# Optimization experiments

Measured on AMD Instinct MI355X. Metric: run time of the kernel, lower is better.

Reference implementation:

```python
import jax, jax.numpy as jnp
import numpy as np

SIGMA = 2.5
B, L, V, C = 8, 2048, 8192, 64
F = 2 * (C + 1)  # top_net in_features = 130


def rbf_interp(points_1, feats_1, points_2, sigma):
    """RBF interpolation of feats_1 at points_1 onto points_2 (atom2D torch_rbf, concat=True).
    points_1: [V,3], feats_1: [V,C], points_2: [L,3] -> [L, C+1]
    """
    # exact cdist via gram trick, [L, V]
    d2 = (jnp.sum(points_2 * points_2, -1)[:, None]
          - 2.0 * (points_2 @ points_1.T)
          + jnp.sum(points_1 * points_1, -1)[None, :])
    d = jnp.sqrt(jnp.maximum(d2, 0.0))
    w = jnp.exp(-d / sigma)                       # [L, V]
    dens = jnp.sum(w, axis=1, keepdims=True)      # [L, 1]
    w = w / dens
    # original computes weights under torch.no_grad()
    w = jax.lax.stop_gradient(w)
    dens = jax.lax.stop_gradient(dens)
    feats_2 = w @ feats_1                         # [L, C]
    return jnp.concatenate([feats_2, dens], axis=1)


def setup_inputs() -> dict:
    key = jax.random.key(0)
    ks = jax.random.split(key, 8)
    return {
        "locs_left": jax.random.normal(ks[0], (B, L, 3), jnp.float32),
        "locs_right": jax.random.normal(ks[1], (B, L, 3), jnp.float32),
        "verts_left": jax.random.normal(ks[2], (B, V, 3), jnp.float32),
        "verts_right": jax.random.normal(ks[3], (B, V, 3), jnp.float32),
        "feats_left": jax.random.normal(ks[4], (B, V, C), jnp.float32),
        "feats_right": jax.random.normal(ks[5], (B, V, C), jnp.float32),
        "w1": jax.random.normal(ks[6], (F, F), jnp.float32) * (1.0 / np.sqrt(F)),
        "b1": jnp.zeros((F,), jnp.float32),
        "w2": jax.random.normal(ks[7], (1, F), jnp.float32) * (1.0 / np.sqrt(F)),
        "b2": jnp.zeros((1,), jnp.float32),
    }


def reference(locs_left, locs_right, verts_left, verts_right,
              feats_left, feats_right, w1, b1, w2, b2):
    interp = jax.vmap(lambda p1, f1, p2: rbf_interp(p1, f1, p2, SIGMA))
    fl = interp(verts_left, feats_left, locs_left)     # [B, L, C+1]
    fr = interp(verts_right, feats_right, locs_right)  # [B, L, C+1]
    x = jnp.concatenate([fl, fr], axis=-1)             # [B, L, 2*(C+1)]
    h = jax.nn.relu(x @ w1.T + b1)                     # dropout inactive at eval
    out = h @ w2.T + b2                                # [B, L, 1]
    return out.reshape(-1)                             # [B*L]
```

## Files before the change

### kernel.cpp

```cpp
#include <hip/hip_runtime.h>
#include <hip/hip_bf16.h>
#include <stdint.h>

#define B_ 8
#define L_ 2048
#define V_ 8192
#define C_ 64
#define F_ 130

typedef float    f32x4  __attribute__((ext_vector_type(4)));
typedef float    f32x2  __attribute__((ext_vector_type(2)));
typedef short    s16x8  __attribute__((ext_vector_type(8)));
typedef __bf16   bf16x8 __attribute__((ext_vector_type(8)));
typedef uint32_t u32x4  __attribute__((ext_vector_type(4)));

#if __has_builtin(__builtin_amdgcn_exp2f)
#define EXP2(x) __builtin_amdgcn_exp2f(x)
#else
#define EXP2(x) exp2f(x)
#endif

#if __has_builtin(__builtin_elementwise_fma)
#define PK_FMA4(a,b,c) __builtin_elementwise_fma((a),(b),(c))
#else
__device__ __forceinline__ f32x4 PK_FMA4(f32x4 a, f32x4 b, f32x4 c) {
  f32x4 r; for (int i=0;i<4;++i) r[i]=fmaf(a[i],b[i],c[i]); return r;
}
#endif
#if __has_builtin(__builtin_elementwise_max)
#define PK_MAX4(a,b) __builtin_elementwise_max((a),(b))
#else
__device__ __forceinline__ f32x4 PK_MAX4(f32x4 a, f32x4 b) {
  f32x4 r; for (int i=0;i<4;++i) r[i]=fmaxf(a[i],b[i]); return r;
}
#endif

constexpr float KEXP2 = (float)(0.57707801635558535 * 0.57707801635558535);

__device__ __forceinline__ uint32_t pack2bf(float a, float b) {
  uint16_t ua = __builtin_bit_cast(uint16_t, (__bf16)a);
  uint16_t ub = __builtin_bit_cast(uint16_t, (__bf16)b);
  return (uint32_t)ua | ((uint32_t)ub << 16);
}

__device__ __forceinline__ float wave_sum(float v) {
  v += __shfl_xor(v, 1);  v += __shfl_xor(v, 2);  v += __shfl_xor(v, 4);
  v += __shfl_xor(v, 8);  v += __shfl_xor(v, 16); v += __shfl_xor(v, 32);
  return v;
}

__device__ __forceinline__ void gload_lds16(const void* g, void* l) {
  __builtin_amdgcn_global_load_lds(
      (const __attribute__((address_space(1))) void*)g,
      (__attribute__((address_space(3))) void*)l, 16, 0, 0);
}

__global__ __launch_bounds__(256) void pre_kernel(
    const float* __restrict__ verts_l, const float* __restrict__ verts_r,
    const float* __restrict__ feats_l, const float* __restrict__ feats_r,
    uint16_t* __restrict__ fT2, float* __restrict__ vS2)
{
  __shared__ float fs[64][68];
  const int blk = blockIdx.x, tid = threadIdx.x;
  if (blk < 1024) {
    const int p = blk >> 6, kt2 = blk & 63;
    const int side = p >> 3, bb = p & 7;
    const float* src = (side ? feats_r : feats_l) + (size_t)bb * (V_ * C_);
    #pragma unroll
    for (int sub = 0; sub < 2; ++sub) {
      const int ktile = kt2 * 2 + sub;
      const int v0 = ktile * 64;
      {
        const int sv = tid >> 2, c0 = (tid & 3) * 16;
        const int m = ((sv >> 3) & 7) << 3;
        const float* s = src + (size_t)(v0 + sv) * C_ + c0;
        f32x4 a = *(const f32x4*)(s);
        f32x4 b = *(const f32x4*)(s + 4);
        f32x4 c = *(const f32x4*)(s + 8);
        f32x4 d = *(const f32x4*)(s + 12);
        *(f32x4*)&fs[sv][(c0)      ^ m] = a;
        *(f32x4*)&fs[sv][(c0 + 4)  ^ m] = b;
        *(f32x4*)&fs[sv][(c0 + 8)  ^ m] = c;
        *(f32x4*)&fs[sv][(c0 + 12) ^ m] = d;
      }
      __syncthreads();
      {
        char* tb = (char*)fT2 + ((size_t)p * 128 + ktile) * 8192;
        #pragma unroll
        for (int half = 0; half < 2; ++half) {
          const int r  = half * 256 + tid;
          const int ch = r >> 3;
          const int kq = (r & 7) ^ (ch & 7);
          const int cs = ch ^ (kq << 3);
          const int row0 = kq * 8;
          float f[8];
          #pragma unroll
          for (int e = 0; e < 8; ++e) f[e] = fs[row0 + e][cs];
          u32x4 val = { pack2bf(f[0], f[1]), pack2bf(f[2], f[3]),
                        pack2bf(f[4], f[5]), pack2bf(f[6], f[7]) };
          *(u32x4*)(tb + r * 16) = val;
        }
      }
      __syncthreads();
    }
  } else {
    const int blk2 = blk - 1024;
    const int p = blk2 >> 5, chunk = blk2 & 31;
    const int side = p >> 3, bb = p & 7;
    const float* src = (side ? verts_r : verts_l) + (size_t)bb * (V_ * 3);
    const int v = chunk * 256 + tid;
    const float x = src[v * 3 + 0], y = src[v * 3 + 1], z = src[v * 3 + 2];
    const float n2 = x * x + y * y + z * z;
    constexpr float M2K = -2.0f * KEXP2;
    float* d = vS2 + (size_t)p * 32768 + (size_t)(v >> 6) * 256 + (v & 63);
    d[0] = M2K * x; d[64] = M2K * y; d[128] = M2K * z; d[192] = KEXP2 * n2;
  }
}

__global__ __launch_bounds__(512, 4) void fused_kernel(
    const float* __restrict__ locs_l, const float* __restrict__ locs_r,
    const uint16_t* __restrict__ fT2, const float* __restrict__ vS2,
    const float* __restrict__ w1, const float* __restrict__ b1,
    const float* __restrict__ w2, const float* __restrict__ b2,
    float* __restrict__ outp)
{
  __shared__ __align__(16) char  flds[3][16384];
  __shared__ __align__(16) float vlds[3][2][4][64];
  __shared__ __align__(16) float xs[32][132];
  __shared__ float densp[32];

  const int bid  = blockIdx.x;
  const int bb   = bid & 7;
  const int tile = bid >> 3;
  const int tid  = threadIdx.x;
  const int wid  = tid >> 6, lane = tid & 63;
  const int g    = wid & 1, h = wid >> 1;
  const int ln15 = lane & 15, lg = lane >> 4;
  const int xorv = (ln15 & 7) << 4;
  const f32x4 zero4 = {0.f, 0.f, 0.f, 0.f};

  const int sub  = h >> 1;
  const int hh   = h & 1;
  const int abfix = sub * 8192 + ln15 * 128 + ((((hh << 2) | lg) << 4) ^ xorv);

  for (int s = 0; s < 2; ++s) {
    const int p = s * 8 + bb;
    const float* locs = (s ? locs_r : locs_l) + (size_t)bb * (L_ * 3);
    const int arow = tile * 32 + g * 16 + ln15;
    const float px = locs[arow * 3 + 0];
    const float py = locs[arow * 3 + 1];
    const float pz = locs[arow * 3 + 2];
    const float pn2p = KEXP2 * (px * px + py * py + pz * pz);
    const f32x4 px4 = {px, px, px, px};
    const f32x4 py4 = {py, py, py, py};
    const f32x4 pz4 = {pz, pz, pz, pz};
    const f32x4 pn4 = {pn2p, pn2p, pn2p, pn2p};

    const char* ftp = (const char*)fT2 + (size_t)p * (128 * 8192);
    const char* vtp = (const char*)vS2 + (size_t)p * (128 * 1024);

    f32x4 acc0 = zero4, acc1 = zero4, acc2 = zero4, acc3 = zero4;
    f32x4 densa = zero4;

    gload_lds16(ftp + wid * 2048 + lane * 16,        &flds[0][wid * 2048]);
    gload_lds16(ftp + wid * 2048 + 1024 + lane * 16, &flds[0][wid * 2048 + 1024]);
    if (wid < 2) gload_lds16(vtp + wid * 1024 + lane * 16, &vlds[0][wid][0][0]);

    const char* gfn = ftp + 16384 + wid * 2048 + lane * 16;
    const char* gvn = vtp + 2048  + wid * 1024 + lane * 16;

    int cur = 0, nxt = 1;
    for (int kt = 0; kt < 64; ++kt) {
      if (kt < 63) {
        gload_lds16(gfn,        &flds[nxt][wid * 2048]);
        gload_lds16(gfn + 1024, &flds[nxt][wid * 2048 + 1024]);
        if (wid < 2) {
          gload_lds16(gvn, &vlds[nxt][wid][0][0]);
          asm volatile("s_waitcnt vmcnt(3)" ::: "memory");
        } else {
          asm volatile("s_waitcnt vmcnt(2)" ::: "memory");
        }
        gfn += 16384;
        gvn += 2048;
      } else {
        asm volatile("s_waitcnt vmcnt(0)" ::: "memory");
      }
      __builtin_amdgcn_s_barrier();

      const int kof = hh * 32 + lg * 8;
      const f32x4 vxa = *(const f32x4*)&vlds[cur][sub][0][kof];
      const f32x4 vxb = *(const f32x4*)&vlds[cur][sub][0][kof + 4];
      const f32x4 vya = *(const f32x4*)&vlds[cur][sub][1][kof];
      const f32x4 vyb = *(const f32x4*)&vlds[cur][sub][1][kof + 4];
      const f32x4 vza = *(const f32x4*)&vlds[cur][sub][2][kof];
      const f32x4 vzb = *(const f32x4*)&vlds[cur][sub][2][kof + 4];
      const f32x4 vna = *(const f32x4*)&vlds[cur][sub][3][kof];
      const f32x4 vnb = *(const f32x4*)&vlds[cur][sub][3][kof + 4];

      f32x4 d2a = PK_FMA4(vza, pz4, vna + pn4);
      d2a = PK_FMA4(vya, py4, d2a);
      d2a = PK_FMA4(vxa, px4, d2a);
      d2a = PK_MAX4(d2a, zero4);
      f32x4 d2b = PK_FMA4(vzb, pz4, vnb + pn4);
      d2b = PK_FMA4(vyb, py4, d2b);
      d2b = PK_FMA4(vxb, px4, d2b);
      d2b = PK_MAX4(d2b, zero4);

      f32x4 wa, wb;
      #pragma unroll
      for (int e = 0; e < 4; ++e) {
        wa[e] = EXP2(-__builtin_amdgcn_sqrtf(d2a[e]));
        wb[e] = EXP2(-__builtin_amdgcn_sqrtf(d2b[e]));
      }
      densa += wa;
      densa += wb;
      bf16x8 av;
      #pragma unroll
      for (int e = 0; e < 4; ++e) {
        av[e]     = (__bf16)wa[e];
        av[e + 4] = (__bf16)wb[e];
      }
      const s16x8 afrag = __builtin_bit_cast(s16x8, av);
      const char* fl = flds[cur];
      const s16x8 bf0 = *(const s16x8*)(fl + abfix);
      const s16x8 bf1 = *(const s16x8*)(fl + abfix + 2048);
      const s16x8 bf2 = *(const s16x8*)(fl + abfix + 4096);
      const s16x8 bf3 = *(const s16x8*)(fl + abfix + 6144);
      acc0 = __builtin_amdgcn_mfma_f32_16x16x32_bf16(afrag, bf0, acc0, 0, 0, 0);
      acc1 = __builtin_amdgcn_mfma_f32_16x16x32_bf16(afrag, bf1, acc1, 0, 0, 0);
      acc2 = __builtin_amdgcn_mfma_f32_16x16x32_bf16(afrag, bf2, acc2, 0, 0, 0);
      acc3 = __builtin_amdgcn_mfma_f32_16x16x32_bf16(afrag, bf3, acc3, 0, 0, 0);

      cur = (cur == 2) ? 0 : cur + 1;
      nxt = (nxt == 2) ? 0 : nxt + 1;
    }

    float dens = (densa.x + densa.y) + (densa.z + densa.w);
    dens += __shfl_xor(dens, 16);
    dens += __shfl_xor(dens, 32);

    #pragma unroll
    for (int ph = 0; ph < 4; ++ph) {
      if (h == ph) {
        if (ph == 0) {
          if (lane < 16) densp[g * 16 + lane] = dens;
          #pragma unroll
          for (int r = 0; r < 4; ++r) {
            const int row = g * 16 + lg * 4 + r;
            xs[row][s * 65 +      ln15] = acc0[r];
            xs[row][s * 65 + 16 + ln15] = acc1[r];
            xs[row][s * 65 + 32 + ln15] = acc2[r];
            xs[row][s * 65 + 48 + ln15] = acc3[r];
          }
        } else {
          if (lane < 16) densp[g * 16 + lane] += dens;
          #pragma unroll
          for (int r = 0; r < 4; ++r) {
            const int row = g * 16 + lg * 4 + r;
            xs[row][s * 65 +      ln15] += acc0[r];
            xs[row][s * 65 + 16 + ln15] += acc1[r];
            xs[row][s * 65 + 32 + ln15] += acc2[r];
            xs[row][s * 65 + 48 + ln15] += acc3[r];
          }
        }
      }
      __syncthreads();
    }
    for (int idx = tid; idx < 32 * 64; idx += 512) {
      const int row = idx >> 6, c = idx & 63;
      xs[row][s * 65 + c] *= (1.0f / densp[row]);
    }
    if (tid < 32) xs[tid][s * 65 + 64] = densp[tid];
    __syncthreads();
  }

  const int r0 = wid * 4;
  float hh0[4] = {0.f,0.f,0.f,0.f}, hh1[4] = {0.f,0.f,0.f,0.f};
  const float* wr0 = w1 + (size_t)lane * F_;
  const float* wr1 = w1 + (size_t)(lane + 64) * F_;

  #pragma unroll 4
  for (int i = 0; i < 128; i += 4) {
    const f32x2 a01 = *(const f32x2*)&wr0[i];
    const f32x2 a23 = *(const f32x2*)&wr0[i + 2];
    const f32x2 c01 = *(const f32x2*)&wr1[i];
    const f32x2 c23 = *(const f32x2*)&wr1[i + 2];
    #pragma unroll
    for (int r = 0; r < 4; ++r) {
      const f32x4 xv = *(const f32x4*)&xs[r0 + r][i];
      hh0[r] = fmaf(xv.x, a01.x, hh0[r]); hh0[r] = fmaf(xv.y, a01.y, hh0[r]);
      hh0[r] = fmaf(xv.z, a23.x, hh0[r]); hh0[r] = fmaf(xv.w, a23.y, hh0[r]);
      hh1[r] = fmaf(xv.x, c01.x, hh1[r]); hh1[r] = fmaf(xv.y, c01.y, hh1[r]);
      hh1[r] = fmaf(xv.z, c23.x, hh1[r]); hh1[r] = fmaf(xv.w, c23.y, hh1[r]);
    }
  }
  {
    const float a0 = wr0[128], a1 = wr0[129];
    const float c0 = wr1[128], c1 = wr1[129];
    #pragma unroll
    for (int r = 0; r < 4; ++r) {
      const float x0 = xs[r0 + r][128], x1 = xs[r0 + r][129];
      hh0[r] = fmaf(x0, a0, fmaf(x1, a1, hh0[r]));
      hh1[r] = fmaf(x0, c0, fmaf(x1, c1, hh1[r]));
    }
  }
  const float* wr2 = w1 + 128 * F_;
  const float* wr3 = w1 + 129 * F_;
  float hp2[4], hp3[4];
  #pragma unroll
  for (int r = 0; r < 4; ++r) {
    const float xa = xs[r0 + r][lane];
    const float xb = xs[r0 + r][lane + 64];
    float p2 = wr2[lane] * xa + wr2[lane + 64] * xb;
    float p3 = wr3[lane] * xa + wr3[lane + 64] * xb;
    if (lane < 2) {
      const float xc = xs[r0 + r][128 + lane];
      p2 += wr2[128 + lane] * xc;
      p3 += wr3[128 + lane] * xc;
    }
    hp2[r] = wave_sum(p2);
    hp3[r] = wave_sum(p3);
  }
  const float b1a = b1[lane], b1b = b1[lane + 64];
  const float w2a = w2[lane], w2b = w2[lane + 64];
  const float b1c = b1[128], b1d = b1[129];
  const float w2c = w2[128], w2d = w2[129];
  const float b2v = b2[0];
  #pragma unroll
  for (int r = 0; r < 4; ++r) {
    float o = w2a * fmaxf(hh0[r] + b1a, 0.f) + w2b * fmaxf(hh1[r] + b1b, 0.f);
    o = wave_sum(o);
    if (lane == 0) {
      o += w2c * fmaxf(hp2[r] + b1c, 0.f) + w2d * fmaxf(hp3[r] + b1d, 0.f);
      outp[(size_t)bb * L_ + tile * 32 + r0 + r] = o + b2v;
    }
  }
}

extern "C" void kernel_launch(void* const* d_in, const int* in_sizes, int n_in,
                              void* d_out, int out_size, void* d_ws, size_t ws_size,
                              hipStream_t stream) {
  const float* locs_l  = (const float*)d_in[0];
  const float* locs_r  = (const float*)d_in[1];
  const float* verts_l = (const float*)d_in[2];
  const float* verts_r = (const float*)d_in[3];
  const float* feats_l = (const float*)d_in[4];
  const float* feats_r = (const float*)d_in[5];
  const float* w1 = (const float*)d_in[6];
  const float* b1 = (const float*)d_in[7];
  const float* w2 = (const float*)d_in[8];
  const float* b2 = (const float*)d_in[9];

  char* ws = (char*)d_ws;
  uint16_t* fT2 = (uint16_t*)ws;
  float*    vS2 = (float*)(ws + 16777216);
  float*    out = (float*)d_out;

  pre_kernel<<<1536, 256, 0, stream>>>(verts_l, verts_r, feats_l, feats_r, fT2, vS2);
  fused_kernel<<<512, 512, 0, stream>>>(locs_l, locs_r, fT2, vS2,
                                        w1, b1, w2, b2, out);
}
```

Baseline: 223.7 us.

## Halve block to 4 waves, each wave computing 32 rows to reuse B fragments

Each block now runs 4 waves instead of 8. Each wave handles both 16-row groups of the 32-row tile, so every LDS-loaded feature fragment feeds two MFMA sets. The per-K-tile staging is redistributed across fewer waves, with more async loads per wave and adjusted waitcnt values, and the MLP epilogue processes 8 rows per wave. This cuts LDS fragment reads and wave count per block. In exchange, each wave holds more accumulator registers and does serial weight generation for two row groups, and occupancy changes through the new launch bounds.

```diff
diff --git a/kernel.cpp b/kernel.cpp
--- a/kernel.cpp
+++ b/kernel.cpp
@@ -117,7 +117,7 @@
   }
 }
 
-__global__ __launch_bounds__(512, 4) void fused_kernel(
+__global__ __launch_bounds__(256, 2) void fused_kernel(
     const float* __restrict__ locs_l, const float* __restrict__ locs_r,
     const uint16_t* __restrict__ fT2, const float* __restrict__ vS2,
     const float* __restrict__ w1, const float* __restrict__ b1,
@@ -134,60 +134,89 @@
   const int tile = bid >> 3;
   const int tid  = threadIdx.x;
   const int wid  = tid >> 6, lane = tid & 63;
-  const int g    = wid & 1, h = wid >> 1;
   const int ln15 = lane & 15, lg = lane >> 4;
   const int xorv = (ln15 & 7) << 4;
   const f32x4 zero4 = {0.f, 0.f, 0.f, 0.f};
 
-  const int sub  = h >> 1;
-  const int hh   = h & 1;
+  const int sub  = wid >> 1;
+  const int hh   = wid & 1;
   const int abfix = sub * 8192 + ln15 * 128 + ((((hh << 2) | lg) << 4) ^ xorv);
+  const int kof  = hh * 32 + lg * 8;
 
   for (int s = 0; s < 2; ++s) {
     const int p = s * 8 + bb;
     const float* locs = (s ? locs_r : locs_l) + (size_t)bb * (L_ * 3);
-    const int arow = tile * 32 + g * 16 + ln15;
-    const float px = locs[arow * 3 + 0];
-    const float py = locs[arow * 3 + 1];
-    const float pz = locs[arow * 3 + 2];
-    const float pn2p = KEXP2 * (px * px + py * py + pz * pz);
-    const f32x4 px4 = {px, px, px, px};
-    const f32x4 py4 = {py, py, py, py};
-    const f32x4 pz4 = {pz, pz, pz, pz};
-    const f32x4 pn4 = {pn2p, pn2p, pn2p, pn2p};
-
-    const char* ftp = (const char*)fT2 + (size_t)p * (128 * 8192);
-    const char* vtp = (const char*)vS2 + (size_t)p * (128 * 1024);
-
-    f32x4 acc0 = zero4, acc1 = zero4, acc2 = zero4, acc3 = zero4;
-    f32x4 densa = zero4;
-
-    gload_lds16(ftp + wid * 2048 + lane * 16,        &flds[0][wid * 2048]);
-    gload_lds16(ftp + wid * 2048 + 1024 + lane * 16, &flds[0][wid * 2048 + 1024]);
-    if (wid < 2) gload_lds16(vtp + wid * 1024 + lane * 16, &vlds[0][wid][0][0]);
-
-    const char* gfn = ftp + 16384 + wid * 2048 + lane * 16;
-    const char* gvn = vtp + 2048  + wid * 1024 + lane * 16;
+    const int arow0 = tile * 32 + ln15;
+    const float qx0 = locs[arow0 * 3 + 0];
+    const float qy0 = locs[arow0 * 3 + 1];
+    const float qz0 = locs[arow0 * 3 + 2];
+    const float qx1 = locs[(arow0 + 16) * 3 + 0];
+    const float qy1 = locs[(arow0 + 16) * 3 + 1];
+    const float qz1 = locs[(arow0 + 16) * 3 + 2];
+    const float qn0 = KEXP2 * (qx0 * qx0 + qy0 * qy0 + qz0 * qz0);
+    const float qn1 = KEXP2 * (qx1 * qx1 + qy1 * qy1 + qz1 * qz1);
+    const f32x4 px0 = {qx0,qx0,qx0,qx0}, py0 = {qy0,qy0,qy0,qy0};
+    const f32x4 pz0 = {qz0,qz0,qz0,qz0}, pn0 = {qn0,qn0,qn0,qn0};
+    const f32x4 px1 = {qx1,qx1,qx1,qx1}, py1 = {qy1,qy1,qy1,qy1};
+    const f32x4 pz1 = {qz1,qz1,qz1,qz1}, pn1 = {qn1,qn1,qn1,qn1};
+
+    const char*  ftp = (const char*)fT2 + (size_t)p * (128 * 8192);
+    const char*  vtp = (const char*)vS2 + (size_t)p * (128 * 1024);
+
+    f32x4 a00 = zero4, a01 = zero4, a02 = zero4, a03 = zero4;
+    f32x4 a10 = zero4, a11 = zero4, a12 = zero4, a13 = zero4;
+    f32x4 dac0 = zero4, dac1 = zero4;
+
+    auto stage = [&](int ktile, int buf) {
+      const char* gf = ftp + (size_t)ktile * 16384 + wid * 1024 + lane * 16;
+      if (wid < 2)
+        gload_lds16(vtp + (size_t)ktile * 2048 + wid * 1024 + lane * 16,
+                    &vlds[buf][wid][0][0]);
+      gload_lds16(gf,         &flds[buf][wid * 1024]);
+      gload_lds16(gf + 4096,  &flds[buf][wid * 1024 + 4096]);
+      gload_lds16(gf + 8192,  &flds[buf][wid * 1024 + 8192]);
+      gload_lds16(gf + 12288, &flds[buf][wid * 1024 + 12288]);
+    };
+
+    auto wgen = [&](const f32x4& vxa, const f32x4& vxb, const f32x4& vya,
+                    const f32x4& vyb, const f32x4& vza, const f32x4& vzb,
+                    const f32x4& vna, const f32x4& vnb,
+                    const f32x4& px4, const f32x4& py4, const f32x4& pz4,
+                    const f32x4& pn4, f32x4& dacc) -> s16x8 {
+      f32x4 d2a = PK_FMA4(vza, pz4, vna + pn4);
+      d2a = PK_FMA4(vya, py4, d2a);
+      d2a = PK_FMA4(vxa, px4, d2a);
+      d2a = PK_MAX4(d2a, zero4);
+      f32x4 d2b = PK_FMA4(vzb, pz4, vnb + pn4);
+      d2b = PK_FMA4(vyb, py4, d2b);
+      d2b = PK_FMA4(vxb, px4, d2b);
+      d2b = PK_MAX4(d2b, zero4);
+      f32x4 wa, wb;
+      #pragma unroll
+      for (int e = 0; e < 4; ++e) {
+        wa[e] = EXP2(-__builtin_amdgcn_sqrtf(d2a[e]));
+        wb[e] = EXP2(-__builtin_amdgcn_sqrtf(d2b[e]));
+      }
+      dacc += wa; dacc += wb;
+      bf16x8 av;
+      #pragma unroll
+      for (int e = 0; e < 4; ++e) { av[e] = (__bf16)wa[e]; av[e+4] = (__bf16)wb[e]; }
+      return __builtin_bit_cast(s16x8, av);
+    };
+
+    stage(0, 0);
 
     int cur = 0, nxt = 1;
     for (int kt = 0; kt < 64; ++kt) {
       if (kt < 63) {
-        gload_lds16(gfn,        &flds[nxt][wid * 2048]);
-        gload_lds16(gfn + 1024, &flds[nxt][wid * 2048 + 1024]);
-        if (wid < 2) {
-          gload_lds16(gvn, &vlds[nxt][wid][0][0]);
-          asm volatile("s_waitcnt vmcnt(3)" ::: "memory");
-        } else {
-          asm volatile("s_waitcnt vmcnt(2)" ::: "memory");
-        }
-        gfn += 16384;
-        gvn += 2048;
+        stage(kt + 1, nxt);
+        if (wid < 2) { asm volatile("s_waitcnt vmcnt(5)" ::: "memory"); }
+        else         { asm volatile("s_waitcnt vmcnt(4)" ::: "memory"); }
       } else {
         asm volatile("s_waitcnt vmcnt(0)" ::: "memory");
       }
       __builtin_amdgcn_s_barrier();
 
-      const int kof = hh * 32 + lg * 8;
       const f32x4 vxa = *(const f32x4*)&vlds[cur][sub][0][kof];
       const f32x4 vxb = *(const f32x4*)&vlds[cur][sub][0][kof + 4];
       const f32x4 vya = *(const f32x4*)&vlds[cur][sub][1][kof];
@@ -197,76 +226,71 @@
       const f32x4 vna = *(const f32x4*)&vlds[cur][sub][3][kof];
       const f32x4 vnb = *(const f32x4*)&vlds[cur][sub][3][kof + 4];
 
-      f32x4 d2a = PK_FMA4(vza, pz4, vna + pn4);
-      d2a = PK_FMA4(vya, py4, d2a);
-      d2a = PK_FMA4(vxa, px4, d2a);
-      d2a = PK_MAX4(d2a, zero4);
-      f32x4 d2b = PK_FMA4(vzb, pz4, vnb + pn4);
-      d2b = PK_FMA4(vyb, py4, d2b);
-      d2b = PK_FMA4(vxb, px4, d2b);
-      d2b = PK_MAX4(d2b, zero4);
-
-      f32x4 wa, wb;
-      #pragma unroll
-      for (int e = 0; e < 4; ++e) {
-        wa[e] = EXP2(-__builtin_amdgcn_sqrtf(d2a[e]));
-        wb[e] = EXP2(-__builtin_amdgcn_sqrtf(d2b[e]));
-      }
-      densa += wa;
-      densa += wb;
-      bf16x8 av;
-      #pragma unroll
-      for (int e = 0; e < 4; ++e) {
-        av[e]     = (__bf16)wa[e];
-        av[e + 4] = (__bf16)wb[e];
-      }
-      const s16x8 afrag = __builtin_bit_cast(s16x8, av);
       const char* fl = flds[cur];
       const s16x8 bf0 = *(const s16x8*)(fl + abfix);
       const s16x8 bf1 = *(const s16x8*)(fl + abfix + 2048);
       const s16x8 bf2 = *(const s16x8*)(fl + abfix + 4096);
       const s16x8 bf3 = *(const s16x8*)(fl + abfix + 6144);
-      acc0 = __builtin_amdgcn_mfma_f32_16x16x32_bf16(afrag, bf0, acc0, 0, 0, 0);
-      acc1 = __builtin_amdgcn_mfma_f32_16x16x32_bf16(afrag, bf1, acc1, 0, 0, 0);
-      acc2 = __builtin_amdgcn_mfma_f32_16x16x32_bf16(afrag, bf2, acc2, 0, 0, 0);
-      acc3 = __builtin_amdgcn_mfma_f32_16x16x32_bf16(afrag, bf3, acc3, 0, 0, 0);
+
+      const s16x8 af0 = wgen(vxa,vxb,vya,vyb,vza,vzb,vna,vnb,
+                             px0,py0,pz0,pn0, dac0);
+      a00 = __builtin_amdgcn_mfma_f32_16x16x32_bf16(af0, bf0, a00, 0, 0, 0);
+      a01 = __builtin_amdgcn_mfma_f32_16x16x32_bf16(af0, bf1, a01, 0, 0, 0);
+      a02 = __builtin_amdgcn_mfma_f32_16x16x32_bf16(af0, bf2, a02, 0, 0, 0);
+      a03 = __builtin_amdgcn_mfma_f32_16x16x32_bf16(af0, bf3, a03, 0, 0, 0);
+
+      const s16x8 af1 = wgen(vxa,vxb,vya,vyb,vza,vzb,vna,vnb,
+                             px1,py1,pz1,pn1, dac1);
+      a10 = __builtin_amdgcn_mfma_f32_16x16x32_bf16(af1, bf0, a10, 0, 0, 0);
+      a11 = __builtin_amdgcn_mfma_f32_16x16x32_bf16(af1, bf1, a11, 0, 0, 0);
+      a12 = __builtin_amdgcn_mfma_f32_16x16x32_bf16(af1, bf2, a12, 0, 0, 0);
+      a13 = __builtin_amdgcn_mfma_f32_16x16x32_bf16(af1, bf3, a13, 0, 0, 0);
 
       cur = (cur == 2) ? 0 : cur + 1;
       nxt = (nxt == 2) ? 0 : nxt + 1;
     }
 
-    float dens = (densa.x + densa.y) + (densa.z + densa.w);
-    dens += __shfl_xor(dens, 16);
-    dens += __shfl_xor(dens, 32);
+    float dens0 = (dac0.x + dac0.y) + (dac0.z + dac0.w);
+    float dens1 = (dac1.x + dac1.y) + (dac1.z + dac1.w);
+    dens0 += __shfl_xor(dens0, 16);  dens0 += __shfl_xor(dens0, 32);
+    dens1 += __shfl_xor(dens1, 16);  dens1 += __shfl_xor(dens1, 32);
 
     #pragma unroll
     for (int ph = 0; ph < 4; ++ph) {
-      if (h == ph) {
+      if (wid == ph) {
         if (ph == 0) {
-          if (lane < 16) densp[g * 16 + lane] = dens;
+          if (lane < 16) { densp[lane] = dens0; densp[16 + lane] = dens1; }
           #pragma unroll
           for (int r = 0; r < 4; ++r) {
-            const int row = g * 16 + lg * 4 + r;
-            xs[row][s * 65 +      ln15] = acc0[r];
-            xs[row][s * 65 + 16 + ln15] = acc1[r];
-            xs[row][s * 65 + 32 + ln15] = acc2[r];
-            xs[row][s * 65 + 48 + ln15] = acc3[r];
+            const int row = lg * 4 + r;
+            xs[row][s * 65 +      ln15] = a00[r];
+            xs[row][s * 65 + 16 + ln15] = a01[r];
+            xs[row][s * 65 + 32 + ln15] = a02[r];
+            xs[row][s * 65 + 48 + ln15] = a03[r];
+            xs[row + 16][s * 65 +      ln15] = a10[r];
+            xs[row + 16][s * 65 + 16 + ln15] = a11[r];
+            xs[row + 16][s * 65 + 32 + ln15] = a12[r];
+            xs[row + 16][s * 65 + 48 + ln15] = a13[r];
           }
         } else {
-          if (lane < 16) densp[g * 16 + lane] += dens;
+          if (lane < 16) { densp[lane] += dens0; densp[16 + lane] += dens1; }
           #pragma unroll
           for (int r = 0; r < 4; ++r) {
-            const int row = g * 16 + lg * 4 + r;
-            xs[row][s * 65 +      ln15] += acc0[r];
-            xs[row][s * 65 + 16 + ln15] += acc1[r];
-            xs[row][s * 65 + 32 + ln15] += acc2[r];
-            xs[row][s * 65 + 48 + ln15] += acc3[r];
+            const int row = lg * 4 + r;
+            xs[row][s * 65 +      ln15] += a00[r];
+            xs[row][s * 65 + 16 + ln15] += a01[r];
+            xs[row][s * 65 + 32 + ln15] += a02[r];
+            xs[row][s * 65 + 48 + ln15] += a03[r];
+            xs[row + 16][s * 65 +      ln15] += a10[r];
+            xs[row + 16][s * 65 + 16 + ln15] += a11[r];
+            xs[row + 16][s * 65 + 32 + ln15] += a12[r];
+            xs[row + 16][s * 65 + 48 + ln15] += a13[r];
           }
         }
       }
       __syncthreads();
     }
-    for (int idx = tid; idx < 32 * 64; idx += 512) {
+    for (int idx = tid; idx < 32 * 64; idx += 256) {
       const int row = idx >> 6, c = idx & 63;
       xs[row][s * 65 + c] *= (1.0f / densp[row]);
     }
@@ -274,19 +298,21 @@
     __syncthreads();
   }
 
-  const int r0 = wid * 4;
-  float hh0[4] = {0.f,0.f,0.f,0.f}, hh1[4] = {0.f,0.f,0.f,0.f};
+  const int r0 = wid * 8;
+  float hh0[8], hh1[8];
+  #pragma unroll
+  for (int r = 0; r < 8; ++r) { hh0[r] = 0.f; hh1[r] = 0.f; }
   const float* wr0 = w1 + (size_t)lane * F_;
   const float* wr1 = w1 + (size_t)(lane + 64) * F_;
 
-  #pragma unroll 4
+  #pragma unroll 2
   for (int i = 0; i < 128; i += 4) {
     const f32x2 a01 = *(const f32x2*)&wr0[i];
     const f32x2 a23 = *(const f32x2*)&wr0[i + 2];
     const f32x2 c01 = *(const f32x2*)&wr1[i];
     const f32x2 c23 = *(const f32x2*)&wr1[i + 2];
     #pragma unroll
-    for (int r = 0; r < 4; ++r) {
+    for (int r = 0; r < 8; ++r) {
       const f32x4 xv = *(const f32x4*)&xs[r0 + r][i];
       hh0[r] = fmaf(xv.x, a01.x, hh0[r]); hh0[r] = fmaf(xv.y, a01.y, hh0[r]);
       hh0[r] = fmaf(xv.z, a23.x, hh0[r]); hh0[r] = fmaf(xv.w, a23.y, hh0[r]);
@@ -298,7 +324,7 @@
     const float a0 = wr0[128], a1 = wr0[129];
     const float c0 = wr1[128], c1 = wr1[129];
     #pragma unroll
-    for (int r = 0; r < 4; ++r) {
+    for (int r = 0; r < 8; ++r) {
       const float x0 = xs[r0 + r][128], x1 = xs[r0 + r][129];
       hh0[r] = fmaf(x0, a0, fmaf(x1, a1, hh0[r]));
       hh1[r] = fmaf(x0, c0, fmaf(x1, c1, hh1[r]));
@@ -306,9 +332,9 @@
   }
   const float* wr2 = w1 + 128 * F_;
   const float* wr3 = w1 + 129 * F_;
-  float hp2[4], hp3[4];
+  float hp2[8], hp3[8];
   #pragma unroll
-  for (int r = 0; r < 4; ++r) {
+  for (int r = 0; r < 8; ++r) {
     const float xa = xs[r0 + r][lane];
     const float xb = xs[r0 + r][lane + 64];
     float p2 = wr2[lane] * xa + wr2[lane + 64] * xb;
@@ -327,7 +353,7 @@
   const float w2c = w2[128], w2d = w2[129];
   const float b2v = b2[0];
   #pragma unroll
-  for (int r = 0; r < 4; ++r) {
+  for (int r = 0; r < 8; ++r) {
     float o = w2a * fmaxf(hh0[r] + b1a, 0.f) + w2b * fmaxf(hh1[r] + b1b, 0.f);
     o = wave_sum(o);
     if (lane == 0) {
@@ -357,6 +383,6 @@
   float*    out = (float*)d_out;
 
   pre_kernel<<<1536, 256, 0, stream>>>(verts_l, verts_r, feats_l, feats_r, fT2, vS2);
-  fused_kernel<<<512, 512, 0, stream>>>(locs_l, locs_r, fT2, vS2,
+  fused_kernel<<<512, 256, 0, stream>>>(locs_l, locs_r, fT2, vS2,
                                         w1, b1, w2, b2, out);
 }
```

After: 224.3 us. Within noise of the previous version (+0.3%).
